# Kernel optimization log

Hardware: AMD Instinct MI355X
Metric: run time of the kernel (lower is better)

The kernel has to match this reference:

```python
import jax, jax.numpy as jnp
import numpy as np

NUM_NODES = 100000
NUM_EDGES = 600000
NUM_GRAPHS = 512
D = 128  # num_features == latent widths


def setup_inputs() -> dict:
    key = jax.random.key(0)
    ks = jax.random.split(key, 16)
    inp = {
        "x": jax.random.normal(ks[0], (NUM_NODES, D), dtype=jnp.float32),
        "edge_index": jax.random.randint(ks[1], (2, NUM_EDGES), 0, NUM_NODES, dtype=jnp.int32),
        "batch": jnp.sort(jax.random.randint(ks[2], (NUM_NODES,), 0, NUM_GRAPHS, dtype=jnp.int32)),
    }
    s = 1.0 / np.sqrt(D)
    # SAGEConv params per layer: lin_l (applied to mean-aggregated neighbors), lin_r (root), bias
    for i in range(3):
        inp[f"Wl{i+1}"] = jax.random.uniform(ks[3 + 3 * i], (D, D), jnp.float32, -s, s)
        inp[f"Wr{i+1}"] = jax.random.uniform(ks[4 + 3 * i], (D, D), jnp.float32, -s, s)
        inp[f"b{i+1}"] = jax.random.uniform(ks[5 + 3 * i], (D,), jnp.float32, -s, s)
    inp["Wro"] = jax.random.uniform(ks[12], (D, 1), jnp.float32, -s, s)
    inp["bro"] = jax.random.uniform(ks[13], (1,), jnp.float32, -s, s)
    return inp


def _sage_conv(h, Wl, Wr, b, src, dst):
    # mean aggregation of source features at destination nodes
    msg = jax.ops.segment_sum(h[src], dst, num_segments=NUM_NODES)          # [N, D]
    cnt = jax.ops.segment_sum(jnp.ones((src.shape[0], 1), h.dtype), dst,
                              num_segments=NUM_NODES)                        # [N, 1]
    mean = msg / jnp.maximum(cnt, 1.0)
    return mean @ Wl + h @ Wr + b


def reference(x, edge_index, batch, Wl1, Wr1, b1, Wl2, Wr2, b2, Wl3, Wr3, b3, Wro, bro):
    src, dst = edge_index[0], edge_index[1]
    h = x
    for Wl, Wr, b in ((Wl1, Wr1, b1), (Wl2, Wr2, b2), (Wl3, Wr3, b3)):
        h = jax.nn.relu(_sage_conv(h, Wl, Wr, b, src, dst))
    # per-graph sum pooling (replaces the python loop over unique batch ids)
    pooled = jax.ops.segment_sum(h, batch, num_segments=NUM_GRAPHS)  # [G, D]
    return jax.nn.sigmoid(pooled @ Wro + bro)  # [G, 1]
```

## Files before the change

### kernel.cpp

```cpp
#include <hip/hip_runtime.h>
#include <math.h>

#define N_NODES 100000
#define N_EDGES 600000
#define N_GRAPHS 512
#define D 128
#define SCAN_BS 1024
#define SCAN_NBC ((N_NODES + SCAN_BS - 1) / SCAN_BS)
#define NPART 8
#define PART_SZ (N_NODES / NPART)
#define E4 (N_EDGES / 4)
#define SPLIT_B 12500

typedef unsigned short u16;
typedef __attribute__((ext_vector_type(8))) short short8;
typedef __attribute__((ext_vector_type(4))) float f32x4;

__device__ __forceinline__ u16 f2bf(float f) {
    unsigned int u = __float_as_uint(f);
    u += 0x7FFFu + ((u >> 16) & 1u);
    return (u16)(u >> 16);
}
__device__ __forceinline__ float bf2f(u16 h) {
    return __uint_as_float(((unsigned int)h) << 16);
}
__device__ __forceinline__ void split2(float f, unsigned int& h16, unsigned int& l16) {
    unsigned int u = __float_as_uint(f);
    unsigned int hb = (u + (0x7FFFu + ((u >> 16) & 1u))) & 0xffff0000u;
    float lo = f - __uint_as_float(hb);
    unsigned int ul = __float_as_uint(lo);
    h16 = hb >> 16;
    l16 = (ul + (0x7FFFu + ((ul >> 16) & 1u))) >> 16;
}

typedef __attribute__((address_space(1))) const unsigned int gas_u32;
typedef __attribute__((address_space(3))) unsigned int las_u32;
__device__ __forceinline__ void gload16(const void* g, void* l) {
    __builtin_amdgcn_global_load_lds((gas_u32*)g, (las_u32*)l, 16, 0, 0);
}

__global__ __launch_bounds__(256) void zero_i_kernel(int* __restrict__ p, int n) {
    int i = blockIdx.x * 256 + threadIdx.x;
    if (i < n) p[i] = 0;
}

__global__ __launch_bounds__(256) void hist_kernel(const int* __restrict__ dst,
                                                   int* __restrict__ deg) {
    int e = blockIdx.x * 256 + threadIdx.x;
    if (e < N_EDGES) atomicAdd(&deg[dst[e]], 1);
}

__global__ __launch_bounds__(1024) void scan1_kernel(const int* __restrict__ deg,
                                                     int* __restrict__ excl,
                                                     int* __restrict__ blocksum) {
    __shared__ int buf[2][SCAN_BS];
    const int t = threadIdx.x;
    const int gid = blockIdx.x * SCAN_BS + t;
    int v = (gid < N_NODES) ? deg[gid] : 0;
    buf[0][t] = v;
    __syncthreads();
    int pi = 0;
    for (int off = 1; off < SCAN_BS; off <<= 1) {
        int val = buf[pi][t];
        if (t >= off) val += buf[pi][t - off];
        buf[pi ^ 1][t] = val;
        pi ^= 1;
        __syncthreads();
    }
    int incl = buf[pi][t];
    if (gid < N_NODES) excl[gid] = incl - v;
    if (t == SCAN_BS - 1) blocksum[blockIdx.x] = incl;
}

__global__ __launch_bounds__(256) void scan3_kernel(const int* __restrict__ excl,
                                                    const int* __restrict__ blocksum,
                                                    int* __restrict__ rowptr) {
    __shared__ int buf[2][128];
    const int t = threadIdx.x;
    if (t < 128) buf[0][t] = (t < SCAN_NBC) ? blocksum[t] : 0;
    __syncthreads();
    int pi = 0;
    for (int off = 1; off < 128; off <<= 1) {
        if (t < 128) {
            int val = buf[pi][t];
            if (t >= off) val += buf[pi][t - off];
            buf[pi ^ 1][t] = val;
        }
        pi ^= 1;
        __syncthreads();
    }
    const int i = blockIdx.x * 256 + t;
    if (i < N_NODES) {
        const int j = i / SCAN_BS;
        const int pref = (j == 0) ? 0 : buf[pi][j - 1];
        rowptr[i] = excl[i] + pref;
    }
    if (i == 0) rowptr[N_NODES] = N_EDGES;
}

__global__ __launch_bounds__(256) void fill_kernel(const int* __restrict__ src,
                                                   const int* __restrict__ dst,
                                                   const int* __restrict__ rowptr,
                                                   int* __restrict__ fill,
                                                   int* __restrict__ csr_src) {
    const int lo = (blockIdx.x & (NPART - 1)) * PART_SZ;
    const int i4 = (blockIdx.x >> 3) * 256 + threadIdx.x;
    if (i4 >= E4) return;
    const int4 d4 = ((const int4*)dst)[i4];
    const int4 s4 = ((const int4*)src)[i4];
    if ((unsigned)(d4.x - lo) < (unsigned)PART_SZ) {
        int pos = rowptr[d4.x] + atomicAdd(&fill[d4.x], 1);
        csr_src[pos] = s4.x;
    }
    if ((unsigned)(d4.y - lo) < (unsigned)PART_SZ) {
        int pos = rowptr[d4.y] + atomicAdd(&fill[d4.y], 1);
        csr_src[pos] = s4.y;
    }
    if ((unsigned)(d4.z - lo) < (unsigned)PART_SZ) {
        int pos = rowptr[d4.z] + atomicAdd(&fill[d4.z], 1);
        csr_src[pos] = s4.z;
    }
    if ((unsigned)(d4.w - lo) < (unsigned)PART_SZ) {
        int pos = rowptr[d4.w] + atomicAdd(&fill[d4.w], 1);
        csr_src[pos] = s4.w;
    }
}

__global__ __launch_bounds__(256) void prep_kernel(const float* __restrict__ x,
                                                   u16* __restrict__ Hhi,
                                                   u16* __restrict__ Hlo,
                                                   const float* __restrict__ Wl1, const float* __restrict__ Wr1,
                                                   const float* __restrict__ Wl2, const float* __restrict__ Wr2,
                                                   const float* __restrict__ Wl3, const float* __restrict__ Wr3,
                                                   u16* __restrict__ wph, u16* __restrict__ wpl) {
    if (blockIdx.x < SPLIT_B) {
        const int i = blockIdx.x * 256 + threadIdx.x;
        const float4 v = ((const float4*)x)[i];
        unsigned int h0, l0, h1, l1, h2, l2, h3, l3;
        split2(v.x, h0, l0); split2(v.y, h1, l1);
        split2(v.z, h2, l2); split2(v.w, h3, l3);
        uint2 oh, ol;
        oh.x = h0 | (h1 << 16); oh.y = h2 | (h3 << 16);
        ol.x = l0 | (l1 << 16); ol.y = l2 | (l3 << 16);
        ((uint2*)Hhi)[i] = oh;
        ((uint2*)Hlo)[i] = ol;
    } else {
        const int b = (blockIdx.x - SPLIT_B) * 4 + (threadIdx.x >> 6);
        const int lane = threadIdx.x & 63;
        const int layer = b >> 6;
        const int t = b & 63;
        const float* Wl = (layer == 0) ? Wl1 : (layer == 1) ? Wl2 : Wl3;
        const float* Wr = (layer == 0) ? Wr1 : (layer == 1) ? Wr2 : Wr3;
        const int nt = t >> 3, kt = t & 7;
        const int n = nt * 16 + (lane & 15);
        const int k0 = kt * 32 + (lane >> 4) * 8;
        const size_t base = (size_t)layer * 32768 + (size_t)(t * 64 + lane) * 8;
        #pragma unroll
        for (int j = 0; j < 8; ++j) {
            const int k = k0 + j;
            const float w = (k < 128) ? Wl[k * 128 + n] : Wr[(k - 128) * 128 + n];
            const u16 h = f2bf(w);
            wph[base + j] = h;
            wpl[base + j] = f2bf(w - bf2f(h));
        }
    }
}

__global__ __launch_bounds__(512, 4) void gemm_kernel(const u16* __restrict__ INhi,
                                                      const u16* __restrict__ INlo,
                                                      const int* __restrict__ rowptr,
                                                      const int* __restrict__ csr_src,
                                                      const u16* __restrict__ Wph,
                                                      const u16* __restrict__ Wpl,
                                                      const float* __restrict__ bias,
                                                      u16* __restrict__ OHhi,
                                                      u16* __restrict__ OHlo,
                                                      const float* __restrict__ Wro,
                                                      float* rowdot) {
    __shared__ uint4 ldsAll[2048];
    const int t = threadIdx.x;
    const int lane = t & 63;
    const int wv = t >> 6;
    const int m0 = blockIdx.x * 128 + wv * 16;
    const int row16 = m0 + (lane & 15);
    int rm = row16; if (rm >= N_NODES) rm = 0;
    const int ko = (lane >> 4) * 8;

    int beg = 0, deg = 0;
    if (row16 < N_NODES) {
        beg = rowptr[row16];
        deg = rowptr[row16 + 1] - beg;
    }

#define STAGE_W(Q, B) do {                                                      \
        const uint4* gh_ = (const uint4*)Wph + (Q) * 512;                       \
        const uint4* gl_ = (const uint4*)Wpl + (Q) * 512;                       \
        gload16(gh_ + t, (void*)&ldsAll[(B) * 1024 + wv * 64]);                 \
        gload16(gl_ + t, (void*)&ldsAll[(B) * 1024 + 512 + wv * 64]);           \
    } while (0)

    STAGE_W(0, 0);
    __builtin_amdgcn_sched_barrier(0);
    STAGE_W(1, 1);
    __builtin_amdgcn_sched_barrier(0);

    short8 ah[4], al[4];
    #pragma unroll
    for (int kt = 0; kt < 4; ++kt) {
        ah[kt] = *(const short8*)(INhi + (size_t)rm * D + kt * 32 + ko);
        al[kt] = *(const short8*)(INlo + (size_t)rm * D + kt * 32 + ko);
    }

    float ac[4][8];
    #pragma unroll
    for (int kt = 0; kt < 4; ++kt) {
        #pragma unroll
        for (int j = 0; j < 8; ++j) ac[kt][j] = 0.f;
    }
    int s_cur = (deg > 0) ? csr_src[beg] : 0;
    for (int n = 0; __any(n < deg); ++n) {
        const bool act = n < deg;
        const int s_nxt = (n + 1 < deg) ? csr_src[beg + n + 1] : 0;
        if (act) {
            const size_t rb = (size_t)s_cur * D + ko;
            #pragma unroll
            for (int kt = 0; kt < 4; ++kt) {
                const uint4 v = *(const uint4*)(INhi + rb + kt * 32);
                ac[kt][0] += __uint_as_float(v.x << 16);
                ac[kt][1] += __uint_as_float(v.x & 0xffff0000u);
                ac[kt][2] += __uint_as_float(v.y << 16);
                ac[kt][3] += __uint_as_float(v.y & 0xffff0000u);
                ac[kt][4] += __uint_as_float(v.z << 16);
                ac[kt][5] += __uint_as_float(v.z & 0xffff0000u);
                ac[kt][6] += __uint_as_float(v.w << 16);
                ac[kt][7] += __uint_as_float(v.w & 0xffff0000u);
            }
        }
        s_cur = s_nxt;
    }
    const float inv = 1.0f / (float)max(deg, 1);
    short8 am[4];
    #pragma unroll
    for (int kt = 0; kt < 4; ++kt) {
        uint4 u;
        u.x = (unsigned)f2bf(ac[kt][0] * inv) | ((unsigned)f2bf(ac[kt][1] * inv) << 16);
        u.y = (unsigned)f2bf(ac[kt][2] * inv) | ((unsigned)f2bf(ac[kt][3] * inv) << 16);
        u.z = (unsigned)f2bf(ac[kt][4] * inv) | ((unsigned)f2bf(ac[kt][5] * inv) << 16);
        u.w = (unsigned)f2bf(ac[kt][6] * inv) | ((unsigned)f2bf(ac[kt][7] * inv) << 16);
        am[kt] = __builtin_bit_cast(short8, u);
    }
    __builtin_amdgcn_sched_barrier(0);

    const int cl = lane & 15;
    const int g4 = (lane >> 4) << 2;

    f32x4 acc8[2][4];

#define COMPUTE_S(Q, B) do {                                                    \
        const u16* bufU_ = (const u16*)(ldsAll + (B) * 1024);                   \
        f32x4 acc_ = {0.f, 0.f, 0.f, 0.f};                                      \
        _Pragma("unroll")                                                       \
        for (int kt_ = 0; kt_ < 8; ++kt_) {                                     \
            const int fo_ = kt_ * 512 + lane * 8;                               \
            const short8 bh_ = *(const short8*)(bufU_ + fo_);                   \
            const short8 bl_ = *(const short8*)(bufU_ + 4096 + fo_);            \
            if (kt_ < 4) {                                                      \
                acc_ = __builtin_amdgcn_mfma_f32_16x16x32_bf16(am[kt_], bh_, acc_, 0, 0, 0); \
                acc_ = __builtin_amdgcn_mfma_f32_16x16x32_bf16(am[kt_], bl_, acc_, 0, 0, 0); \
            } else {                                                            \
                acc_ = __builtin_amdgcn_mfma_f32_16x16x32_bf16(ah[kt_ - 4], bh_, acc_, 0, 0, 0); \
                acc_ = __builtin_amdgcn_mfma_f32_16x16x32_bf16(ah[kt_ - 4], bl_, acc_, 0, 0, 0); \
                acc_ = __builtin_amdgcn_mfma_f32_16x16x32_bf16(al[kt_ - 4], bh_, acc_, 0, 0, 0); \
            }                                                                   \
        }                                                                       \
        acc8[(Q) >> 2][(Q) & 3] = acc_;                                         \
    } while (0)

    asm volatile("s_waitcnt vmcnt(0)" ::: "memory");
    __builtin_amdgcn_s_barrier();
    COMPUTE_S(0, 0);
    __builtin_amdgcn_s_barrier();
    STAGE_W(2, 0);
    __builtin_amdgcn_sched_barrier(0);
    COMPUTE_S(1, 1);
    __builtin_amdgcn_s_barrier();
    STAGE_W(3, 1);
    asm volatile("s_waitcnt vmcnt(2)" ::: "memory");
    __builtin_amdgcn_s_barrier();
    COMPUTE_S(2, 0);
    __builtin_amdgcn_s_barrier();
    STAGE_W(4, 0);
    asm volatile("s_waitcnt vmcnt(2)" ::: "memory");
    __builtin_amdgcn_s_barrier();
    COMPUTE_S(3, 1);
    __builtin_amdgcn_s_barrier();
    STAGE_W(5, 1);
    asm volatile("s_waitcnt vmcnt(2)" ::: "memory");
    __builtin_amdgcn_s_barrier();
    COMPUTE_S(4, 0);
    __builtin_amdgcn_s_barrier();
    STAGE_W(6, 0);
    asm volatile("s_waitcnt vmcnt(2)" ::: "memory");
    __builtin_amdgcn_s_barrier();
    COMPUTE_S(5, 1);
    __builtin_amdgcn_s_barrier();
    STAGE_W(7, 1);
    asm volatile("s_waitcnt vmcnt(2)" ::: "memory");
    __builtin_amdgcn_s_barrier();
    COMPUTE_S(6, 0);
    asm volatile("s_waitcnt vmcnt(0)" ::: "memory");
    __builtin_amdgcn_s_barrier();
    COMPUTE_S(7, 1);

    char* bounceB = (char*)ldsAll + wv * 2048;

    if (rowdot) {
        float wsum[4] = {0.f, 0.f, 0.f, 0.f};
        #pragma unroll
        for (int si = 0; si < 2; ++si) {
            #pragma unroll
            for (int nt2 = 0; nt2 < 4; ++nt2) {
                const int col = (si * 4 + nt2) * 16 + cl;
                const float bv = bias[col];
                const float wroc = Wro[col];
                #pragma unroll
                for (int r = 0; r < 4; ++r) {
                    const float v = fmaxf(acc8[si][nt2][r] + bv, 0.f);
                    wsum[r] = fmaf(v, wroc, wsum[r]);
                }
            }
        }
        #pragma unroll
        for (int r = 0; r < 4; ++r) {
            float tsum = wsum[r];
            tsum += __shfl_down(tsum, 8, 64);
            tsum += __shfl_down(tsum, 4, 64);
            tsum += __shfl_down(tsum, 2, 64);
            tsum += __shfl_down(tsum, 1, 64);
            const int row = m0 + g4 + r;
            if (cl == 0 && row < N_NODES) {
                rowdot[row] = tsum;
            }
        }
    } else {
        #pragma unroll
        for (int si = 0; si < 2; ++si) {
            asm volatile("s_waitcnt lgkmcnt(0)" ::: "memory");
            unsigned int lo_pack[8];
            #pragma unroll
            for (int nt2 = 0; nt2 < 4; ++nt2) {
                const int col = (si * 4 + nt2) * 16 + cl;
                const float bv = bias[col];
                #pragma unroll
                for (int r = 0; r < 4; ++r) {
                    const int rr = g4 + r;
                    const float v = fmaxf(acc8[si][nt2][r] + bv, 0.f);
                    unsigned int h16, l16;
                    split2(v, h16, l16);
                    const int boff = (rr * 128 + (nt2 * 16 + cl) * 2) ^ ((rr & 7) << 4);
                    *(u16*)(bounceB + boff) = (u16)h16;
                    if (r & 1) lo_pack[nt2 * 2 + (r >> 1)] |= l16 << 16;
                    else       lo_pack[nt2 * 2 + (r >> 1)]  = l16;
                }
            }
            asm volatile("s_waitcnt lgkmcnt(0)" ::: "memory");
            #pragma unroll
            for (int j = 0; j < 2; ++j) {
                const int rr = j * 8 + (lane >> 3);
                const int blk = lane & 7;
                const uint4 vv = *(const uint4*)(bounceB + rr * 128 + ((blk ^ (rr & 7)) << 4));
                const int grow = m0 + rr;
                if (grow < N_NODES)
                    *(uint4*)(OHhi + (size_t)grow * D + si * 64 + blk * 8) = vv;
            }
            asm volatile("s_waitcnt lgkmcnt(0)" ::: "memory");
            #pragma unroll
            for (int nt2 = 0; nt2 < 4; ++nt2) {
                #pragma unroll
                for (int r = 0; r < 4; ++r) {
                    const int rr = g4 + r;
                    const unsigned int l16 = (lo_pack[nt2 * 2 + (r >> 1)] >> ((r & 1) * 16)) & 0xffffu;
                    const int boff = (rr * 128 + (nt2 * 16 + cl) * 2) ^ ((rr & 7) << 4);
                    *(u16*)(bounceB + boff) = (u16)l16;
                }
            }
            asm volatile("s_waitcnt lgkmcnt(0)" ::: "memory");
            #pragma unroll
            for (int j = 0; j < 2; ++j) {
                const int rr = j * 8 + (lane >> 3);
                const int blk = lane & 7;
                const uint4 vv = *(const uint4*)(bounceB + rr * 128 + ((blk ^ (rr & 7)) << 4));
                const int grow = m0 + rr;
                if (grow < N_NODES)
                    *(uint4*)(OHlo + (size_t)grow * D + si * 64 + blk * 8) = vv;
            }
        }
    }
#undef STAGE_W
#undef COMPUTE_S
}

__global__ __launch_bounds__(64) void final_kernel(const float* __restrict__ rowdot,
                                                   const int* __restrict__ batch,
                                                   const float* __restrict__ bro,
                                                   float* __restrict__ out) {
    const int g = blockIdx.x;
    const int t = threadIdx.x;
    int lo = 0, hi = N_NODES;
    while (lo < hi) { int mid = (lo + hi) >> 1; if (batch[mid] < g) lo = mid + 1; else hi = mid; }
    int lo2 = lo, hi2 = N_NODES;
    while (lo2 < hi2) { int mid = (lo2 + hi2) >> 1; if (batch[mid] < g + 1) lo2 = mid + 1; else hi2 = mid; }

    float acc = 0.0f;
    for (int i = lo + t; i < lo2; i += 64) acc += rowdot[i];
    #pragma unroll
    for (int off = 32; off > 0; off >>= 1) acc += __shfl_down(acc, off, 64);
    if (t == 0) out[g] = 1.0f / (1.0f + expf(-(acc + bro[0])));
}

extern "C" void kernel_launch(void* const* d_in, const int* in_sizes, int n_in,
                              void* d_out, int out_size, void* d_ws, size_t ws_size,
                              hipStream_t stream) {
    const float* x     = (const float*)d_in[0];
    const int*   ei    = (const int*)d_in[1];
    const int*   batch = (const int*)d_in[2];
    const int*   src   = ei;
    const int*   dst   = ei + N_EDGES;
    const float* Wl[3] = {(const float*)d_in[3], (const float*)d_in[6], (const float*)d_in[9]};
    const float* Wr[3] = {(const float*)d_in[4], (const float*)d_in[7], (const float*)d_in[10]};
    const float* bs[3] = {(const float*)d_in[5], (const float*)d_in[8], (const float*)d_in[11]};
    const float* Wro   = (const float*)d_in[12];
    const float* bro   = (const float*)d_in[13];
    float* out = (float*)d_out;

    const size_t ND = (size_t)N_NODES * D;
    char* ws = (char*)d_ws;
    u16* Ahi = (u16*)ws;
    u16* Alo = Ahi + ND;
    u16* Bhi = Alo + ND;
    u16* Blo = Bhi + ND;
    u16* Wph = Blo + ND;
    u16* Wpl = Wph + 3 * 32768;
    int* deg      = (int*)(Wpl + 3 * 32768);
    int* fill     = deg + N_NODES;
    float* rowdot = (float*)(fill + N_NODES);
    int* excl     = (int*)(rowdot + N_NODES);
    int* blocksum = excl + N_NODES;
    int* rowptr   = blocksum + 128;
    int* csr_src  = rowptr + N_NODES + 1;

    const int EB      = (N_EDGES + 255) / 256;
    const int NB      = (N_NODES + 255) / 256;
    const int NB2     = (2 * N_NODES + 255) / 256;
    const int EPB     = ((E4 + 255) / 256) * NPART;
    const int PREP_B  = SPLIT_B + 48;
    const int GEMM_B  = (N_NODES + 127) / 128;

    zero_i_kernel<<<NB2, 256, 0, stream>>>(deg, 2 * N_NODES);
    hist_kernel<<<EB, 256, 0, stream>>>(dst, deg);
    scan1_kernel<<<SCAN_NBC, SCAN_BS, 0, stream>>>(deg, excl, blocksum);
    scan3_kernel<<<NB, 256, 0, stream>>>(excl, blocksum, rowptr);
    fill_kernel<<<EPB, 256, 0, stream>>>(src, dst, rowptr, fill, csr_src);

    prep_kernel<<<PREP_B, 256, 0, stream>>>(x, Ahi, Alo,
                                            Wl[0], Wr[0], Wl[1], Wr[1], Wl[2], Wr[2],
                                            Wph, Wpl);

    gemm_kernel<<<GEMM_B, 512, 0, stream>>>(Ahi, Alo, rowptr, csr_src,
                                            Wph, Wpl, bs[0],
                                            Bhi, Blo, Wro, (float*)nullptr);
    gemm_kernel<<<GEMM_B, 512, 0, stream>>>(Bhi, Blo, rowptr, csr_src,
                                            Wph + 32768, Wpl + 32768, bs[1],
                                            Ahi, Alo, Wro, (float*)nullptr);
    gemm_kernel<<<GEMM_B, 512, 0, stream>>>(Ahi, Alo, rowptr, csr_src,
                                            Wph + 2 * 32768, Wpl + 2 * 32768, bs[2],
                                            Bhi, Blo, Wro, rowdot);

    final_kernel<<<N_GRAPHS, 64, 0, stream>>>(rowdot, batch, bro, out);
}
```

Baseline: 362.2 us.

## Sort nodes by in-degree so each GEMM tile gathers balanced neighbor counts

Adds a counting sort of nodes by in-degree (per-block histogram, single-block scan, stable scatter) to build a permutation. Each fused aggregate+GEMM kernel then processes rows in permuted order, so the 16 rows in a wave have similar degrees and gather loops diverge less. In exchange, input-row reads and output-row writes become scattered through the permutation, which costs locality, and three small kernels are added to the launch sequence.

```diff
diff --git a/kernel.cpp b/kernel.cpp
--- a/kernel.cpp
+++ b/kernel.cpp
@@ -11,6 +11,8 @@
 #define PART_SZ (N_NODES / NPART)
 #define E4 (N_EDGES / 4)
 #define SPLIT_B 12500
+#define DBINS 64
+#define DNB ((N_NODES + 255) / 256)
 
 typedef unsigned short u16;
 typedef __attribute__((ext_vector_type(8))) short short8;
@@ -123,6 +125,64 @@
     if ((unsigned)(d4.w - lo) < (unsigned)PART_SZ) {
         int pos = rowptr[d4.w] + atomicAdd(&fill[d4.w], 1);
         csr_src[pos] = s4.w;
+    }
+}
+
+__global__ __launch_bounds__(256) void dhist_kernel(const int* __restrict__ deg,
+                                                    int* __restrict__ histT) {
+    __shared__ int h[DBINS];
+    const int t = threadIdx.x;
+    if (t < DBINS) h[t] = 0;
+    __syncthreads();
+    const int i = blockIdx.x * 256 + t;
+    if (i < N_NODES) {
+        const int b = 63 - min(deg[i], 63);
+        atomicAdd(&h[b], 1);
+    }
+    __syncthreads();
+    if (t < DBINS) histT[t * DNB + blockIdx.x] = h[t];
+}
+
+__global__ __launch_bounds__(1024) void dscan_kernel(int* __restrict__ histT) {
+    __shared__ int buf[2][1024];
+    const int t = threadIdx.x;
+    const int TOT = DBINS * DNB;
+    const int CH = (TOT + 1023) / 1024;
+    const int base = t * CH;
+    int s = 0;
+    for (int k = 0; k < CH; ++k) {
+        const int idx = base + k;
+        if (idx < TOT) s += histT[idx];
+    }
+    buf[0][t] = s;
+    __syncthreads();
+    int pi = 0;
+    for (int off = 1; off < 1024; off <<= 1) {
+        int val = buf[pi][t];
+        if (t >= off) val += buf[pi][t - off];
+        buf[pi ^ 1][t] = val;
+        pi ^= 1;
+        __syncthreads();
+    }
+    int pref = (t == 0) ? 0 : buf[pi][t - 1];
+    for (int k = 0; k < CH; ++k) {
+        const int idx = base + k;
+        if (idx < TOT) { const int v = histT[idx]; histT[idx] = pref; pref += v; }
+    }
+}
+
+__global__ __launch_bounds__(256) void dscatter_kernel(const int* __restrict__ deg,
+                                                       const int* __restrict__ offs,
+                                                       int* __restrict__ perm) {
+    __shared__ int c[DBINS];
+    const int t = threadIdx.x;
+    if (t < DBINS) c[t] = 0;
+    __syncthreads();
+    const int i = blockIdx.x * 256 + t;
+    if (i < N_NODES) {
+        const int b = 63 - min(deg[i], 63);
+        const int r = atomicAdd(&c[b], 1);
+        perm[offs[b * DNB + blockIdx.x] + r] = i;
     }
 }
 
@@ -170,6 +230,7 @@
                                                       const u16* __restrict__ INlo,
                                                       const int* __restrict__ rowptr,
                                                       const int* __restrict__ csr_src,
+                                                      const int* __restrict__ perm,
                                                       const u16* __restrict__ Wph,
                                                       const u16* __restrict__ Wpl,
                                                       const float* __restrict__ bias,
@@ -182,15 +243,16 @@
     const int lane = t & 63;
     const int wv = t >> 6;
     const int m0 = blockIdx.x * 128 + wv * 16;
-    const int row16 = m0 + (lane & 15);
-    int rm = row16; if (rm >= N_NODES) rm = 0;
+    const int gid = m0 + (lane & 15);
     const int ko = (lane >> 4) * 8;
 
-    int beg = 0, deg = 0;
-    if (row16 < N_NODES) {
-        beg = rowptr[row16];
-        deg = rowptr[row16 + 1] - beg;
-    }
+    int prow = 0, beg = 0, deg = 0;
+    if (gid < N_NODES) {
+        prow = perm[gid];
+        beg = rowptr[prow];
+        deg = rowptr[prow + 1] - beg;
+    }
+    const int rm = prow;
 
 #define STAGE_W(Q, B) do {                                                      \
         const uint4* gh_ = (const uint4*)Wph + (Q) * 512;                       \
@@ -337,9 +399,9 @@
             tsum += __shfl_down(tsum, 4, 64);
             tsum += __shfl_down(tsum, 2, 64);
             tsum += __shfl_down(tsum, 1, 64);
-            const int row = m0 + g4 + r;
-            if (cl == 0 && row < N_NODES) {
-                rowdot[row] = tsum;
+            const int lg = m0 + g4 + r;
+            if (cl == 0 && lg < N_NODES) {
+                rowdot[perm[lg]] = tsum;
             }
         }
     } else {
@@ -369,9 +431,9 @@
                 const int rr = j * 8 + (lane >> 3);
                 const int blk = lane & 7;
                 const uint4 vv = *(const uint4*)(bounceB + rr * 128 + ((blk ^ (rr & 7)) << 4));
-                const int grow = m0 + rr;
-                if (grow < N_NODES)
-                    *(uint4*)(OHhi + (size_t)grow * D + si * 64 + blk * 8) = vv;
+                const int lg = m0 + rr;
+                if (lg < N_NODES)
+                    *(uint4*)(OHhi + (size_t)perm[lg] * D + si * 64 + blk * 8) = vv;
             }
             asm volatile("s_waitcnt lgkmcnt(0)" ::: "memory");
             #pragma unroll
@@ -390,9 +452,9 @@
                 const int rr = j * 8 + (lane >> 3);
                 const int blk = lane & 7;
                 const uint4 vv = *(const uint4*)(bounceB + rr * 128 + ((blk ^ (rr & 7)) << 4));
-                const int grow = m0 + rr;
-                if (grow < N_NODES)
-                    *(uint4*)(OHlo + (size_t)grow * D + si * 64 + blk * 8) = vv;
+                const int lg = m0 + rr;
+                if (lg < N_NODES)
+                    *(uint4*)(OHlo + (size_t)perm[lg] * D + si * 64 + blk * 8) = vv;
             }
         }
     }
@@ -448,6 +510,8 @@
     int* blocksum = excl + N_NODES;
     int* rowptr   = blocksum + 128;
     int* csr_src  = rowptr + N_NODES + 1;
+    int* histT    = csr_src + N_EDGES;
+    int* perm     = histT + DBINS * DNB;
 
     const int EB      = (N_EDGES + 255) / 256;
     const int NB      = (N_NODES + 255) / 256;
@@ -462,17 +526,21 @@
     scan3_kernel<<<NB, 256, 0, stream>>>(excl, blocksum, rowptr);
     fill_kernel<<<EPB, 256, 0, stream>>>(src, dst, rowptr, fill, csr_src);
 
+    dhist_kernel<<<DNB, 256, 0, stream>>>(deg, histT);
+    dscan_kernel<<<1, 1024, 0, stream>>>(histT);
+    dscatter_kernel<<<DNB, 256, 0, stream>>>(deg, histT, perm);
+
     prep_kernel<<<PREP_B, 256, 0, stream>>>(x, Ahi, Alo,
                                             Wl[0], Wr[0], Wl[1], Wr[1], Wl[2], Wr[2],
                                             Wph, Wpl);
 
-    gemm_kernel<<<GEMM_B, 512, 0, stream>>>(Ahi, Alo, rowptr, csr_src,
+    gemm_kernel<<<GEMM_B, 512, 0, stream>>>(Ahi, Alo, rowptr, csr_src, perm,
                                             Wph, Wpl, bs[0],
                                             Bhi, Blo, Wro, (float*)nullptr);
-    gemm_kernel<<<GEMM_B, 512, 0, stream>>>(Bhi, Blo, rowptr, csr_src,
+    gemm_kernel<<<GEMM_B, 512, 0, stream>>>(Bhi, Blo, rowptr, csr_src, perm,
                                             Wph + 32768, Wpl + 32768, bs[1],
                                             Ahi, Alo, Wro, (float*)nullptr);
-    gemm_kernel<<<GEMM_B, 512, 0, stream>>>(Ahi, Alo, rowptr, csr_src,
+    gemm_kernel<<<GEMM_B, 512, 0, stream>>>(Ahi, Alo, rowptr, csr_src, perm,
                                             Wph + 2 * 32768, Wpl + 2 * 32768, bs[2],
                                             Bhi, Blo, Wro, rowdot);
 
```

Measured after the change: 369.9 us. +2.1%, slower.
